# Performance work log

Hardware: AMD Instinct MI355X
Metric: run time of the kernel (lower is better)

The kernel has to match this reference:

```python
import jax, jax.numpy as jnp
import numpy as np

D_MODEL = 1024
N_HEADS = 16
HEAD_DIM = D_MODEL // N_HEADS
D_FF = 4096
EPS = 1e-5


def layer_norm(x, w, b):
    mu = jnp.mean(x, axis=-1, keepdims=True)
    var = jnp.var(x, axis=-1, keepdims=True)
    return (x - mu) * jax.lax.rsqrt(var + EPS) * w + b


def setup_inputs() -> dict:
    key = jax.random.key(0)
    ks = jax.random.split(key, 8)
    B, T, C = 2, 2048, D_MODEL
    s = lambda fan_in: 1.0 / np.sqrt(fan_in)
    return {
        "x": jax.random.normal(ks[0], (B, T, C), dtype=jnp.float32),
        "ln1_w": jnp.ones((C,), jnp.float32),
        "ln1_b": jnp.zeros((C,), jnp.float32),
        "qkv_w": jax.random.normal(ks[1], (3 * C, C), jnp.float32) * s(C),
        "attn_out_w": jax.random.normal(ks[2], (C, C), jnp.float32) * s(C),
        "ln2_w": jnp.ones((C,), jnp.float32),
        "ln2_b": jnp.zeros((C,), jnp.float32),
        "mlp_in_w": jax.random.normal(ks[3], (D_FF, C), jnp.float32) * s(C),
        "mlp_gate_w": jax.random.normal(ks[4], (D_FF, C), jnp.float32) * s(C),
        "mlp_out_w": jax.random.normal(ks[5], (C, D_FF), jnp.float32) * s(D_FF),
    }


def reference(x, ln1_w, ln1_b, qkv_w, attn_out_w, ln2_w, ln2_b,
              mlp_in_w, mlp_gate_w, mlp_out_w):
    B, T, C = x.shape
    # --- causal self-attention (pre-norm) ---
    h = layer_norm(x, ln1_w, ln1_b)
    qkv = h @ qkv_w.T  # [B,T,3C]
    q, k, v = jnp.split(qkv, 3, axis=-1)
    def heads(t):
        return t.reshape(B, T, N_HEADS, HEAD_DIM).transpose(0, 2, 1, 3)  # [B,H,T,Dh]
    q, k, v = heads(q), heads(k), heads(v)
    scale = HEAD_DIM ** -0.5
    scores = jnp.einsum("bhqd,bhkd->bhqk", q, k) * scale  # [B,H,T,T]
    causal = jnp.tril(jnp.ones((T, T), dtype=bool))
    scores = jnp.where(causal, scores, -jnp.inf)
    attn = jax.nn.softmax(scores, axis=-1)
    out = jnp.einsum("bhqk,bhkd->bhqd", attn, v)
    out = out.transpose(0, 2, 1, 3).reshape(B, T, C)
    x = x + out @ attn_out_w.T
    # --- SwiGLU MLP (pre-norm) ---
    h = layer_norm(x, ln2_w, ln2_b)
    acts = jax.nn.silu(h @ mlp_in_w.T) * (h @ mlp_gate_w.T)
    return x + acts @ mlp_out_w.T
```

## Files before the change

### kernel.cpp

```cpp
#include <hip/hip_runtime.h>
#include <cstdint>

typedef unsigned short u16;
typedef __bf16 bf16x8 __attribute__((ext_vector_type(8)));
typedef float  f32x4  __attribute__((ext_vector_type(4)));

struct alignas(16) F4 { float v[4]; };
struct alignas(8)  U4 { u16 v[4]; };
struct alignas(16) U8 { u16 v[8]; };

__device__ __forceinline__ u16 f2bf(float f) {
    union { float f; unsigned int u; } x; x.f = f;
    unsigned int r = x.u + 0x7fffu + ((x.u >> 16) & 1u);
    return (u16)(r >> 16);
}
__device__ __forceinline__ float bf2f(u16 u) {
    union { unsigned int u; float f; } x; x.u = ((unsigned int)u) << 16;
    return x.f;
}
__device__ __forceinline__ f32x4 mfma16(bf16x8 a, bf16x8 b, f32x4 c) {
    return __builtin_amdgcn_mfma_f32_16x16x32_bf16(a, b, c, 0, 0, 0);
}
__device__ __forceinline__ bf16x8 ldf(const u16* p) { return *(const bf16x8*)p; }
__device__ __forceinline__ void gload_lds16(const void* g, void* l) {
    auto* gp = reinterpret_cast<const __attribute__((address_space(1))) unsigned int*>(
        reinterpret_cast<uintptr_t>(g));
    auto* lp = reinterpret_cast<__attribute__((address_space(3))) unsigned int*>(
        reinterpret_cast<uintptr_t>(l));
    __builtin_amdgcn_global_load_lds(gp, lp, 16, 0, 0);
}

__global__ __launch_bounds__(256) void cast_bf16_k(const float* __restrict__ in,
                                                   u16* __restrict__ out, int n4) {
    int i = blockIdx.x * 256 + threadIdx.x;
    if (i >= n4) return;
    F4 v = *(const F4*)(in + (size_t)i * 4);
    U4 o;
    #pragma unroll
    for (int j = 0; j < 4; ++j) o.v[j] = f2bf(v.v[j]);
    *(U4*)(out + (size_t)i * 4) = o;
}

__global__ __launch_bounds__(256) void cast_wig_k(const float* __restrict__ wi,
                                                  const float* __restrict__ wg,
                                                  u16* __restrict__ wig) {
    int i = blockIdx.x * 256 + threadIdx.x;
    const int w  = i >> 7;
    const int c8 = (i & 127) * 8;
    const int f  = ((w >> 6) << 5) | (w & 31);
    const float* src = ((w & 32) ? wg : wi) + (size_t)f * 1024 + c8;
    F4 a = *(const F4*)src;
    F4 b = *(const F4*)(src + 4);
    U8 o;
    #pragma unroll
    for (int j = 0; j < 4; ++j) { o.v[j] = f2bf(a.v[j]); o.v[4 + j] = f2bf(b.v[j]); }
    *(U8*)(wig + (size_t)w * 1024 + c8) = o;
}

__global__ __launch_bounds__(256) void ln_fwd_k(const float* __restrict__ x,
                                                const float* __restrict__ w,
                                                const float* __restrict__ b,
                                                u16* __restrict__ h) {
    const int row = blockIdx.x, tid = threadIdx.x;
    const float* xr = x + (size_t)row * 1024;
    F4 v = *(const F4*)(xr + tid * 4);
    float s  = v.v[0] + v.v[1] + v.v[2] + v.v[3];
    float ss = v.v[0]*v.v[0] + v.v[1]*v.v[1] + v.v[2]*v.v[2] + v.v[3]*v.v[3];
    #pragma unroll
    for (int o = 32; o > 0; o >>= 1) { s += __shfl_down(s, o); ss += __shfl_down(ss, o); }
    __shared__ float red[8];
    const int wave = tid >> 6, lane = tid & 63;
    if (lane == 0) { red[wave] = s; red[4 + wave] = ss; }
    __syncthreads();
    s  = red[0] + red[1] + red[2] + red[3];
    ss = red[4] + red[5] + red[6] + red[7];
    const float mu   = s * (1.0f / 1024.0f);
    const float var  = ss * (1.0f / 1024.0f) - mu * mu;
    const float rstd = rsqrtf(var + 1e-5f);
    U4 o;
    #pragma unroll
    for (int j = 0; j < 4; ++j)
        o.v[j] = f2bf((v.v[j] - mu) * rstd * w[tid * 4 + j] + b[tid * 4 + j]);
    *(U4*)(h + (size_t)row * 1024 + tid * 4) = o;
}

template <int MODE>
__global__ __launch_bounds__(256) void gemm_bt_k(const u16* __restrict__ A,
                                                 const u16* __restrict__ Bm,
                                                 void* __restrict__ Cout,
                                                 const float* __restrict__ resid,
                                                 int M, int N, int K) {
    __shared__ u16 Alds[128 * 32];
    __shared__ u16 Blds[128 * 32];
    const int tid  = threadIdx.x;
    const int lane = tid & 63, wave = tid >> 6;
    const int wr = wave >> 1, wc = wave & 1;
    const int r16 = lane & 15, g16 = lane >> 4;
    const int bn = blockIdx.x, bm = blockIdx.y;

    const int srow = lane >> 2;
    const int scol = (lane & 3) * 8;

    f32x4 acc[4][4] = {};

    for (int k0 = 0; k0 < K; k0 += 32) {
        #pragma unroll
        for (int c = 0; c < 2; ++c) {
            const int ch = wave * 2 + c;
            const u16* ga = A  + ((size_t)bm * 128 + ch * 16 + srow) * K + k0 + scol;
            gload_lds16(ga, &Alds[ch * 512]);
            const u16* gb = Bm + ((size_t)bn * 128 + ch * 16 + srow) * K + k0 + scol;
            gload_lds16(gb, &Blds[ch * 512]);
        }
        __syncthreads();
        bf16x8 af[4], bfr[4];
        #pragma unroll
        for (int m = 0; m < 4; ++m)
            af[m] = *(const bf16x8*)&Alds[(wr * 64 + m * 16 + r16) * 32 + g16 * 8];
        #pragma unroll
        for (int n = 0; n < 4; ++n)
            bfr[n] = *(const bf16x8*)&Blds[(wc * 64 + n * 16 + r16) * 32 + g16 * 8];
        #pragma unroll
        for (int m = 0; m < 4; ++m)
            #pragma unroll
            for (int n = 0; n < 4; ++n)
                acc[m][n] = mfma16(af[m], bfr[n], acc[m][n]);
        __syncthreads();
    }

    #pragma unroll
    for (int m = 0; m < 4; ++m) {
        #pragma unroll
        for (int n = 0; n < 4; ++n) {
            #pragma unroll
            for (int r = 0; r < 4; ++r) {
                const int row = bm * 128 + wr * 64 + m * 16 + g16 * 4 + r;
                const int col = bn * 128 + wc * 64 + n * 16 + r16;
                const float v = acc[m][n][r];
                if (MODE == 0) {
                    ((u16*)Cout)[(size_t)row * N + col] = f2bf(v);
                } else {
                    ((float*)Cout)[(size_t)row * N + col] =
                        resid[(size_t)row * N + col] + v;
                }
            }
        }
    }
}

template <int EPI>
__global__ __launch_bounds__(512, 2)
void gemm256_k(const u16* __restrict__ A, const u16* __restrict__ Bm,
               void* __restrict__ Cout, int lda, int ldb, int kLen,
               int nx, int bnCh, int outLd, int planeEls) {
    __shared__ u16 lds[2][2][2][128 * 64];

    const int tid  = threadIdx.x;
    const int wave = tid >> 6, lane = tid & 63;
    const int wm = wave >> 2, wn = wave & 3;
    const int r16 = lane & 15, g16 = lane >> 4;

    const int cpx = gridDim.x >> 3;
    const int xcd = blockIdx.x & 7, loc = blockIdx.x >> 3;
    const int mCh = cpx / bnCh;
    const int cpr = nx / bnCh;
    const int bm = (xcd / cpr) * mCh + loc / bnCh;
    const int bn = (xcd % cpr) * bnCh + loc % bnCh;
    const int kBeg = blockIdx.z * kLen;
    const int NT = kLen >> 6;

    const int wr0 = wave * 16 + (lane >> 3);
    const int csw = ((lane & 7) ^ (lane >> 3)) * 8;
    const u16* aP[2][2]; const u16* bP[2][2];
    #pragma unroll
    for (int h = 0; h < 2; ++h) {
        #pragma unroll
        for (int i = 0; i < 2; ++i) {
            const int wr = wr0 + i * 8;
            const int ar = (wr >> 6) * 128 + h * 64 + (wr & 63);
            const int br = (wr >> 5) * 64 + h * 32 + (wr & 31);
            aP[h][i] = A  + (size_t)(bm * 256 + ar) * lda + kBeg + csw;
            bP[h][i] = Bm + (size_t)(bn * 256 + br) * ldb + kBeg + csw;
        }
    }

    auto stA = [&](int kt, int h) {
        u16* d = &lds[kt & 1][0][h][wave * 1024];
        gload_lds16(aP[h][0] + kt * 64, d);
        gload_lds16(aP[h][1] + kt * 64, d + 512);
    };
    auto stB = [&](int kt, int h) {
        u16* d = &lds[kt & 1][1][h][wave * 1024];
        gload_lds16(bP[h][0] + kt * 64, d);
        gload_lds16(bP[h][1] + kt * 64, d + 512);
    };

    int offA[4][2], offB[2][2];
    #pragma unroll
    for (int m = 0; m < 4; ++m)
        #pragma unroll
        for (int ks = 0; ks < 2; ++ks)
            offA[m][ks] = (wm * 64 + m * 16 + r16) * 64 + (((ks * 4 + g16) ^ (r16 & 7)) * 8);
    #pragma unroll
    for (int n = 0; n < 2; ++n)
        #pragma unroll
        for (int ks = 0; ks < 2; ++ks)
            offB[n][ks] = (wn * 32 + n * 16 + r16) * 64 + (((ks * 4 + g16) ^ (r16 & 7)) * 8);

    f32x4 acc[8][4] = {};

    stA(0, 0); stB(0, 0); stB(0, 1); stA(0, 1);
    stA(1, 0); stB(1, 0); stB(1, 1); stA(1, 1);
    asm volatile("s_waitcnt vmcnt(8)" ::: "memory");
    __builtin_amdgcn_s_barrier();

    for (int kt = 0; kt < NT; ++kt) {
        const int buf = kt & 1;
        const u16* A0 = &lds[buf][0][0][0];
        const u16* A1 = &lds[buf][0][1][0];
        const u16* B0 = &lds[buf][1][0][0];
        const u16* B1 = &lds[buf][1][1][0];
        const bool pf = (kt + 2 < NT);
        bf16x8 af[4][2], b0[2][2], b1[2][2];

        #pragma unroll
        for (int m = 0; m < 4; ++m) {
            af[m][0] = ldf(A0 + offA[m][0]);
            af[m][1] = ldf(A0 + offA[m][1]);
        }
        #pragma unroll
        for (int n = 0; n < 2; ++n) {
            b0[n][0] = ldf(B0 + offB[n][0]);
            b0[n][1] = ldf(B0 + offB[n][1]);
        }
        __builtin_amdgcn_s_setprio(1);
        #pragma unroll
        for (int m = 0; m < 4; ++m)
            #pragma unroll
            for (int n = 0; n < 2; ++n) {
                acc[m][n] = mfma16(af[m][0], b0[n][0], acc[m][n]);
                acc[m][n] = mfma16(af[m][1], b0[n][1], acc[m][n]);
            }
        __builtin_amdgcn_s_setprio(0);
        __builtin_amdgcn_s_barrier();

        #pragma unroll
        for (int n = 0; n < 2; ++n) {
            b1[n][0] = ldf(B1 + offB[n][0]);
            b1[n][1] = ldf(B1 + offB[n][1]);
        }
        if (pf) { stA(kt + 2, 0); stB(kt + 2, 0); }
        __builtin_amdgcn_s_setprio(1);
        #pragma unroll
        for (int m = 0; m < 4; ++m)
            #pragma unroll
            for (int n = 0; n < 2; ++n) {
                acc[m][n + 2] = mfma16(af[m][0], b1[n][0], acc[m][n + 2]);
                acc[m][n + 2] = mfma16(af[m][1], b1[n][1], acc[m][n + 2]);
            }
        __builtin_amdgcn_s_setprio(0);
        __builtin_amdgcn_s_barrier();

        #pragma unroll
        for (int m = 0; m < 4; ++m) {
            af[m][0] = ldf(A1 + offA[m][0]);
            af[m][1] = ldf(A1 + offA[m][1]);
        }
        if (pf) stB(kt + 2, 1);
        __builtin_amdgcn_s_setprio(1);
        #pragma unroll
        for (int m = 0; m < 4; ++m)
            #pragma unroll
            for (int n = 0; n < 2; ++n) {
                acc[m + 4][n] = mfma16(af[m][0], b0[n][0], acc[m + 4][n]);
                acc[m + 4][n] = mfma16(af[m][1], b0[n][1], acc[m + 4][n]);
            }
        __builtin_amdgcn_s_setprio(0);
        __builtin_amdgcn_s_barrier();

        if (pf) stA(kt + 2, 1);
        __builtin_amdgcn_s_setprio(1);
        #pragma unroll
        for (int m = 0; m < 4; ++m)
            #pragma unroll
            for (int n = 0; n < 2; ++n) {
                acc[m + 4][n + 2] = mfma16(af[m][0], b1[n][0], acc[m + 4][n + 2]);
                acc[m + 4][n + 2] = mfma16(af[m][1], b1[n][1], acc[m + 4][n + 2]);
            }
        __builtin_amdgcn_s_setprio(0);
        if (pf)                   { asm volatile("s_waitcnt vmcnt(8)" ::: "memory"); }
        else if (kt + 1 < NT)     { asm volatile("s_waitcnt vmcnt(0)" ::: "memory"); }
        if (kt + 1 < NT) __builtin_amdgcn_s_barrier();
    }

    if constexpr (EPI == 1) {
        float* P = (float*)Cout + (size_t)blockIdx.z * planeEls;
        #pragma unroll
        for (int m = 0; m < 8; ++m) {
            #pragma unroll
            for (int n = 0; n < 4; ++n) {
                #pragma unroll
                for (int r = 0; r < 4; ++r) {
                    const int row = bm * 256 + wm * 128 + m * 16 + g16 * 4 + r;
                    const int col = bn * 256 + wn * 64 + n * 16 + r16;
                    P[(size_t)row * outLd + col] = acc[m][n][r];
                }
            }
        }
    } else {
        (void)planeEls;
        u16* O = (u16*)Cout;
        #pragma unroll
        for (int m = 0; m < 8; ++m) {
            #pragma unroll
            for (int n = 0; n < 2; ++n) {
                #pragma unroll
                for (int r = 0; r < 4; ++r) {
                    const int row = bm * 256 + wm * 128 + m * 16 + g16 * 4 + r;
                    const int col = (bn * 4 + wn) * 32 + n * 16 + r16;
                    const float vi = acc[m][n][r];
                    const float vg = acc[m][n + 2][r];
                    const float sl = vi / (1.0f + __expf(-vi));
                    O[(size_t)row * outLd + col] = f2bf(sl * vg);
                }
            }
        }
    }
}

__global__ __launch_bounds__(256) void addreduce4_k(const float* __restrict__ resid,
                                                    const float* __restrict__ p,
                                                    float* __restrict__ out,
                                                    int n4, int planeEls) {
    for (int i = blockIdx.x * 256 + threadIdx.x; i < n4; i += gridDim.x * 256) {
        F4 a = *(const F4*)(resid + (size_t)i * 4);
        F4 b = *(const F4*)(p + (size_t)i * 4);
        F4 c = *(const F4*)(p + (size_t)planeEls + (size_t)i * 4);
        F4 d = *(const F4*)(p + (size_t)2 * planeEls + (size_t)i * 4);
        F4 e = *(const F4*)(p + (size_t)3 * planeEls + (size_t)i * 4);
        F4 o;
        #pragma unroll
        for (int j = 0; j < 4; ++j) o.v[j] = a.v[j] + b.v[j] + c.v[j] + d.v[j] + e.v[j];
        *(F4*)(out + (size_t)i * 4) = o;
    }
}

__global__ __launch_bounds__(256) void attn_fwd_k(const u16* __restrict__ qk,
                                                  const u16* __restrict__ vt,
                                                  u16* __restrict__ Ob) {
    __shared__ u16 Klds[2][64 * 64];
    __shared__ u16 Vlds[2][64 * 64];

    const int tid  = threadIdx.x;
    const int wave = tid >> 6, lane = tid & 63;
    const int r16  = lane & 15, g16 = lane >> 4;

    const int blk = blockIdx.x;
    const int xcd = blk & 7;
    const int pc  = blk >> 3;
    const int hh  = pc >> 5;
    const int qb  = (31 - (pc & 31) + 8 * hh) & 31;
    const int bh  = xcd * 4 + hh;
    const int h   = bh & 15, b = bh >> 4;

    const int q0w = qb * 64 + wave * 16;
    const size_t seqb = (size_t)b * 2048;

    const u16* qp = qk + (seqb + q0w + r16) * 2048 + h * 64 + g16 * 8;
    const bf16x8 qf0 = *(const bf16x8*)qp;
    const bf16x8 qf1 = *(const bf16x8*)(qp + 32);

    const u16* kbase = qk + seqb * 2048 + 1024 + (size_t)h * 64;
    const u16* vbase = vt + (size_t)(h * 64) * 4096 + seqb;

    const int srow  = tid >> 3;
    const int scol8 = ((tid & 7) ^ (srow & 7)) * 8;
    const u16* ksrc = kbase + (size_t)srow * 2048 + scol8;
    const u16* vsrc = vbase + (size_t)srow * 4096 + scol8;

    auto stage = [&](int bufi, int kv0) {
        const u16* kp = ksrc + (size_t)kv0 * 2048;
        const u16* vp = vsrc + kv0;
        u16* kd = &Klds[bufi][wave * 512];
        u16* vd = &Vlds[bufi][wave * 512];
        gload_lds16(kp, kd);
        gload_lds16(kp + (size_t)32 * 2048, kd + 2048);
        gload_lds16(vp, vd);
        gload_lds16(vp + (size_t)32 * 4096, vd + 2048);
    };

    f32x4 o[4] = {};
    float mreg = -3.0e38f, lreg = 0.0f;
    constexpr float SC = 0.125f * 1.44269504088896341f;

    const int nt = qb + 1;
    stage(0, 0);
    asm volatile("s_waitcnt vmcnt(0)" ::: "memory");
    __builtin_amdgcn_s_barrier();

    for (int it = 0; it < nt; ++it) {
        const int kv0 = it * 64;
        const int cur = it & 1;
        if (it + 1 < nt) stage(cur ^ 1, kv0 + 64);

        const u16* K = Klds[cur];
        const u16* V = Vlds[cur];

        f32x4 s[4];
        #pragma unroll
        for (int t = 0; t < 4; ++t) {
            const int row = 16 * t + r16;
            const int sw  = row & 7;
            const bf16x8 k0 = *(const bf16x8*)&K[row * 64 + ((g16 ^ sw) * 8)];
            const bf16x8 k1 = *(const bf16x8*)&K[row * 64 + (((g16 + 4) ^ sw) * 8)];
            f32x4 acc = {0.f, 0.f, 0.f, 0.f};
            acc = mfma16(k0, qf0, acc);
            acc = mfma16(k1, qf1, acc);
            s[t] = acc;
        }

        float a[16];
        #pragma unroll
        for (int t = 0; t < 4; ++t)
            #pragma unroll
            for (int r = 0; r < 4; ++r) a[4 * t + r] = s[t][r] * SC;

        if (kv0 + 63 > q0w) {
            const int qg = q0w + r16;
            #pragma unroll
            for (int t = 0; t < 4; ++t)
                #pragma unroll
                for (int r = 0; r < 4; ++r)
                    if (kv0 + 16 * t + 4 * g16 + r > qg) a[4 * t + r] = -1.0e30f;
        }

        float mx = a[0];
        #pragma unroll
        for (int j = 1; j < 16; ++j) mx = fmaxf(mx, a[j]);
        mx = fmaxf(mx, __shfl_xor(mx, 16));
        mx = fmaxf(mx, __shfl_xor(mx, 32));
        const float mn = fmaxf(mreg, mx);
        const float al = exp2f(mreg - mn);
        float p[16], rs = 0.0f;
        #pragma unroll
        for (int j = 0; j < 16; ++j) { p[j] = exp2f(a[j] - mn); rs += p[j]; }
        rs += __shfl_xor(rs, 16);
        rs += __shfl_xor(rs, 32);
        lreg = lreg * al + rs;
        mreg = mn;

        bf16x8 pf0, pf1;
        #pragma unroll
        for (int j = 0; j < 8; ++j) { pf0[j] = (__bf16)p[j]; pf1[j] = (__bf16)p[8 + j]; }

        #pragma unroll
        for (int t = 0; t < 4; ++t) {
            const int row  = 16 * t + r16;
            const int sw   = row & 7;
            const int base = row * 64 + (g16 & 1) * 4;
            const int c0   = g16 >> 1;
            U4 a0 = *(const U4*)&V[base + (((c0 + 0) ^ sw) * 8)];
            U4 a1 = *(const U4*)&V[base + (((c0 + 2) ^ sw) * 8)];
            U4 b0 = *(const U4*)&V[base + (((c0 + 4) ^ sw) * 8)];
            U4 b1 = *(const U4*)&V[base + (((c0 + 6) ^ sw) * 8)];
            #pragma unroll
            for (int r = 0; r < 4; ++r) o[t][r] *= al;
            bf16x8 v0, v1;
            #pragma unroll
            for (int j = 0; j < 4; ++j) {
                v0[j]     = ((const __bf16*)&a0)[j];
                v0[4 + j] = ((const __bf16*)&a1)[j];
                v1[j]     = ((const __bf16*)&b0)[j];
                v1[4 + j] = ((const __bf16*)&b1)[j];
            }
            o[t] = mfma16(v0, pf0, o[t]);
            o[t] = mfma16(v1, pf1, o[t]);
        }

        if (it + 1 < nt) {
            asm volatile("s_waitcnt vmcnt(0)" ::: "memory");
            __builtin_amdgcn_s_barrier();
        }
    }

    const float inv = 1.0f / lreg;
    u16* op = Ob + (seqb + q0w + r16) * 1024 + h * 64 + 4 * g16;
    #pragma unroll
    for (int t = 0; t < 4; ++t) {
        U4 st;
        #pragma unroll
        for (int r = 0; r < 4; ++r) st.v[r] = f2bf(o[t][r] * inv);
        *(U4*)(op + 16 * t) = st;
    }
}

extern "C" void kernel_launch(void* const* d_in, const int* in_sizes, int n_in,
                              void* d_out, int out_size, void* d_ws, size_t ws_size,
                              hipStream_t stream) {
    (void)in_sizes; (void)n_in; (void)out_size; (void)ws_size;
    constexpr int C = 1024, FF = 4096, M = 2 * 2048;
    constexpr size_t MB = 1024 * 1024;

    const float* x      = (const float*)d_in[0];
    const float* ln1_w  = (const float*)d_in[1];
    const float* ln1_b  = (const float*)d_in[2];
    const float* qkv_w  = (const float*)d_in[3];
    const float* atto_w = (const float*)d_in[4];
    const float* ln2_w  = (const float*)d_in[5];
    const float* ln2_b  = (const float*)d_in[6];
    const float* mlpi_w = (const float*)d_in[7];
    const float* mlpg_w = (const float*)d_in[8];
    const float* mlpo_w = (const float*)d_in[9];
    float* out = (float*)d_out;

    char* ws = (char*)d_ws;
    size_t off = 0;
    auto alloc = [&](size_t bytes) {
        char* p = ws + off;
        off += (bytes + 255) & ~(size_t)255;
        return p;
    };
    u16*   wq   = (u16*)  alloc((size_t)3 * C * C * 2);
    u16*   wo   = (u16*)  alloc((size_t)C * C * 2);
    u16*   wig  = (u16*)  alloc((size_t)2 * FF * C * 2);
    u16*   wm   = (u16*)  alloc((size_t)C * FF * 2);
    float* x1   = (float*)alloc((size_t)M * C * 4);
    u16*   h2   = (u16*)  alloc((size_t)M * C * 2);
    u16*   ab   = (u16*)  alloc((size_t)M * FF * 2);
    char*  R    = alloc(64 * MB);
    u16*   h1   = (u16*)R;
    u16*   qk_b = (u16*)(R + 8 * MB);
    u16*   vt_b = (u16*)(R + 24 * MB);
    u16*   Ob   = (u16*)(R + 32 * MB);
    float* pscr = (float*)R;

    cast_bf16_k<<<(3 * C * C / 4) / 256, 256, 0, stream>>>(qkv_w, wq, 3 * C * C / 4);
    cast_bf16_k<<<(C * C / 4) / 256, 256, 0, stream>>>(atto_w, wo, C * C / 4);
    cast_bf16_k<<<(C * FF / 4) / 256, 256, 0, stream>>>(mlpo_w, wm, C * FF / 4);
    cast_wig_k<<<(2 * FF * C / 8) / 256, 256, 0, stream>>>(mlpi_w, mlpg_w, wig);

    ln_fwd_k<<<M, 256, 0, stream>>>(x, ln1_w, ln1_b, h1);
    gemm_bt_k<0><<<dim3(2 * C / 128, M / 128), 256, 0, stream>>>(h1, wq, qk_b, nullptr, M, 2 * C, C);
    const u16* wv = wq + (size_t)2 * C * C;
    gemm_bt_k<0><<<dim3(M / 128, C / 128), 256, 0, stream>>>(wv, h1, vt_b, nullptr, C, M, C);
    attn_fwd_k<<<1024, 256, 0, stream>>>(qk_b, vt_b, Ob);
    gemm_bt_k<1><<<dim3(C / 128, M / 128), 256, 0, stream>>>(Ob, wo, x1, x, M, C, C);

    ln_fwd_k<<<M, 256, 0, stream>>>(x1, ln2_w, ln2_b, h2);
    gemm256_k<2><<<dim3((2 * FF / 256) * (M / 256), 1, 1), 512, 0, stream>>>(
        h2, wig, ab, C, C, C, 2 * FF / 256, 8, FF, 0);
    gemm256_k<1><<<dim3((C / 256) * (M / 256), 1, 4), 512, 0, stream>>>(
        ab, wm, pscr, FF, FF, FF / 4, C / 256, 4, C, M * C);
    addreduce4_k<<<2048, 256, 0, stream>>>(x1, pscr, out, M * C / 4, M * C);
}
```

Baseline: 297.4 us.

## Software-pipeline LDS fragment reads across k-iterations in GEMM main loop

Restructures the bf16 MFMA GEMM main loop so the LDS reads of A and B fragments for the next k-tile are issued during the current tile's last MFMA group, not at the start of each quadrant. It keeps separate register sets for both A halves and both B halves. It also replaces the four precomputed global pointers per operand with one base pointer plus 32-bit offsets, which cuts 64-bit address registers. The point is to hide LDS latency behind matrix-core work. In exchange it raises VGPR pressure, which could lower occupancy or cause spills.

New measurement: 293.9 us. About the same (-1.2%).

```diff
diff --git a/kernel.cpp b/kernel.cpp
--- a/kernel.cpp
+++ b/kernel.cpp
@@ -169,30 +169,31 @@
     const int kBeg = blockIdx.z * kLen;
     const int NT = kLen >> 6;
 
-    const int wr0 = wave * 16 + (lane >> 3);
     const int csw = ((lane & 7) ^ (lane >> 3)) * 8;
-    const u16* aP[2][2]; const u16* bP[2][2];
+    const u16* aU = A  + (size_t)(bm * 256) * lda + kBeg;
+    const u16* bU = Bm + (size_t)(bn * 256) * ldb + kBeg;
+    int aOff[2][2], bOff[2][2];
     #pragma unroll
     for (int h = 0; h < 2; ++h) {
         #pragma unroll
         for (int i = 0; i < 2; ++i) {
-            const int wr = wr0 + i * 8;
+            const int wr = wave * 16 + (lane >> 3) + i * 8;
             const int ar = (wr >> 6) * 128 + h * 64 + (wr & 63);
             const int br = (wr >> 5) * 64 + h * 32 + (wr & 31);
-            aP[h][i] = A  + (size_t)(bm * 256 + ar) * lda + kBeg + csw;
-            bP[h][i] = Bm + (size_t)(bn * 256 + br) * ldb + kBeg + csw;
+            aOff[h][i] = ar * lda + csw;
+            bOff[h][i] = br * ldb + csw;
         }
     }
 
     auto stA = [&](int kt, int h) {
         u16* d = &lds[kt & 1][0][h][wave * 1024];
-        gload_lds16(aP[h][0] + kt * 64, d);
-        gload_lds16(aP[h][1] + kt * 64, d + 512);
+        gload_lds16(aU + aOff[h][0] + kt * 64, d);
+        gload_lds16(aU + aOff[h][1] + kt * 64, d + 512);
     };
     auto stB = [&](int kt, int h) {
         u16* d = &lds[kt & 1][1][h][wave * 1024];
-        gload_lds16(bP[h][0] + kt * 64, d);
-        gload_lds16(bP[h][1] + kt * 64, d + 512);
+        gload_lds16(bU + bOff[h][0] + kt * 64, d);
+        gload_lds16(bU + bOff[h][1] + kt * 64, d + 512);
     };
 
     int offA[4][2], offB[2][2];
@@ -208,89 +209,103 @@
             offB[n][ks] = (wn * 32 + n * 16 + r16) * 64 + (((ks * 4 + g16) ^ (r16 & 7)) * 8);
 
     f32x4 acc[8][4] = {};
+    bf16x8 af0[4][2], af1[4][2], b0v[2][2], b1v[2][2];
+
+    auto rdAF0 = [&](int buf) {
+        const u16* P = &lds[buf][0][0][0];
+        #pragma unroll
+        for (int m = 0; m < 4; ++m) {
+            af0[m][0] = ldf(P + offA[m][0]);
+            af0[m][1] = ldf(P + offA[m][1]);
+        }
+    };
+    auto rdAF1 = [&](int buf) {
+        const u16* P = &lds[buf][0][1][0];
+        #pragma unroll
+        for (int m = 0; m < 4; ++m) {
+            af1[m][0] = ldf(P + offA[m][0]);
+            af1[m][1] = ldf(P + offA[m][1]);
+        }
+    };
+    auto rdB0 = [&](int buf) {
+        const u16* P = &lds[buf][1][0][0];
+        #pragma unroll
+        for (int n = 0; n < 2; ++n) {
+            b0v[n][0] = ldf(P + offB[n][0]);
+            b0v[n][1] = ldf(P + offB[n][1]);
+        }
+    };
+    auto rdB1 = [&](int buf) {
+        const u16* P = &lds[buf][1][1][0];
+        #pragma unroll
+        for (int n = 0; n < 2; ++n) {
+            b1v[n][0] = ldf(P + offB[n][0]);
+            b1v[n][1] = ldf(P + offB[n][1]);
+        }
+    };
 
     stA(0, 0); stB(0, 0); stB(0, 1); stA(0, 1);
     stA(1, 0); stB(1, 0); stB(1, 1); stA(1, 1);
     asm volatile("s_waitcnt vmcnt(8)" ::: "memory");
     __builtin_amdgcn_s_barrier();
+    rdAF0(0); rdB0(0); rdB1(0); rdAF1(0);
 
     for (int kt = 0; kt < NT; ++kt) {
-        const int buf = kt & 1;
-        const u16* A0 = &lds[buf][0][0][0];
-        const u16* A1 = &lds[buf][0][1][0];
-        const u16* B0 = &lds[buf][1][0][0];
-        const u16* B1 = &lds[buf][1][1][0];
         const bool pf = (kt + 2 < NT);
-        bf16x8 af[4][2], b0[2][2], b1[2][2];
-
-        #pragma unroll
-        for (int m = 0; m < 4; ++m) {
-            af[m][0] = ldf(A0 + offA[m][0]);
-            af[m][1] = ldf(A0 + offA[m][1]);
-        }
-        #pragma unroll
-        for (int n = 0; n < 2; ++n) {
-            b0[n][0] = ldf(B0 + offB[n][0]);
-            b0[n][1] = ldf(B0 + offB[n][1]);
-        }
+        const int nb = (kt + 1) & 1;
+
         __builtin_amdgcn_s_setprio(1);
         #pragma unroll
         for (int m = 0; m < 4; ++m)
             #pragma unroll
             for (int n = 0; n < 2; ++n) {
-                acc[m][n] = mfma16(af[m][0], b0[n][0], acc[m][n]);
-                acc[m][n] = mfma16(af[m][1], b0[n][1], acc[m][n]);
+                acc[m][n] = mfma16(af0[m][0], b0v[n][0], acc[m][n]);
+                acc[m][n] = mfma16(af0[m][1], b0v[n][1], acc[m][n]);
             }
         __builtin_amdgcn_s_setprio(0);
         __builtin_amdgcn_s_barrier();
 
-        #pragma unroll
-        for (int n = 0; n < 2; ++n) {
-            b1[n][0] = ldf(B1 + offB[n][0]);
-            b1[n][1] = ldf(B1 + offB[n][1]);
-        }
         if (pf) { stA(kt + 2, 0); stB(kt + 2, 0); }
         __builtin_amdgcn_s_setprio(1);
         #pragma unroll
         for (int m = 0; m < 4; ++m)
             #pragma unroll
             for (int n = 0; n < 2; ++n) {
-                acc[m][n + 2] = mfma16(af[m][0], b1[n][0], acc[m][n + 2]);
-                acc[m][n + 2] = mfma16(af[m][1], b1[n][1], acc[m][n + 2]);
+                acc[m][n + 2] = mfma16(af0[m][0], b1v[n][0], acc[m][n + 2]);
+                acc[m][n + 2] = mfma16(af0[m][1], b1v[n][1], acc[m][n + 2]);
             }
         __builtin_amdgcn_s_setprio(0);
         __builtin_amdgcn_s_barrier();
 
-        #pragma unroll
-        for (int m = 0; m < 4; ++m) {
-            af[m][0] = ldf(A1 + offA[m][0]);
-            af[m][1] = ldf(A1 + offA[m][1]);
-        }
         if (pf) stB(kt + 2, 1);
         __builtin_amdgcn_s_setprio(1);
         #pragma unroll
         for (int m = 0; m < 4; ++m)
             #pragma unroll
             for (int n = 0; n < 2; ++n) {
-                acc[m + 4][n] = mfma16(af[m][0], b0[n][0], acc[m + 4][n]);
-                acc[m + 4][n] = mfma16(af[m][1], b0[n][1], acc[m + 4][n]);
+                acc[m + 4][n] = mfma16(af1[m][0], b0v[n][0], acc[m + 4][n]);
+                acc[m + 4][n] = mfma16(af1[m][1], b0v[n][1], acc[m + 4][n]);
             }
         __builtin_amdgcn_s_setprio(0);
         __builtin_amdgcn_s_barrier();
 
         if (pf) stA(kt + 2, 1);
+        if (pf)               { asm volatile("s_waitcnt vmcnt(8)" ::: "memory"); }
+        else if (kt + 1 < NT) { asm volatile("s_waitcnt vmcnt(0)" ::: "memory"); }
+        if (kt + 1 < NT) {
+            __builtin_amdgcn_s_barrier();
+            rdAF0(nb); rdB0(nb);
+        }
         __builtin_amdgcn_s_setprio(1);
         #pragma unroll
         for (int m = 0; m < 4; ++m)
             #pragma unroll
             for (int n = 0; n < 2; ++n) {
-                acc[m + 4][n + 2] = mfma16(af[m][0], b1[n][0], acc[m + 4][n + 2]);
-                acc[m + 4][n + 2] = mfma16(af[m][1], b1[n][1], acc[m + 4][n + 2]);
+                acc[m + 4][n + 2] = mfma16(af1[m][0], b1v[n][0], acc[m + 4][n + 2]);
+                acc[m + 4][n + 2] = mfma16(af1[m][1], b1v[n][1], acc[m + 4][n + 2]);
             }
         __builtin_amdgcn_s_setprio(0);
-        if (pf)                   { asm volatile("s_waitcnt vmcnt(8)" ::: "memory"); }
-        else if (kt + 1 < NT)     { asm volatile("s_waitcnt vmcnt(0)" ::: "memory"); }
-        if (kt + 1 < NT) __builtin_amdgcn_s_barrier();
+        if (kt + 1 < NT) { rdB1(nb); rdAF1(nb); }
     }
 
     if constexpr (EPI == 1) {
```
